# Kernel optimization log

Measured on AMD Instinct MI355X. Metric: run time of the kernel, lower is better.

Reference implementation:

```python
import jax, jax.numpy as jnp
import numpy as np
from jax import lax

ACT_BITS = 8
O, C, K = 256, 128, 3
STRIDE, PAD = 1, 1


def setup_inputs() -> dict:
    key = jax.random.key(0)
    kx, kw = jax.random.split(key)
    x = jax.random.uniform(kx, (16, C, 56, 56), dtype=jnp.float32)
    weight = jax.random.normal(kw, (O, C, K, K), dtype=jnp.float32)
    wrange = 2 ** 8  # weight_bits
    qw = jnp.clip(jnp.round(weight * (wrange - 1)), 0, wrange - 1)
    # PCILT: pcilt[o,c,kh,kw,i] = qw[o,c,kh,kw] * i  for i in [0, 2^act_bits)
    A = 2 ** ACT_BITS
    pcilt = qw[..., None] * jnp.arange(A, dtype=jnp.float32)  # [O,C,K,K,A]
    bias = jnp.zeros((O,), dtype=jnp.float32)
    return {"x": x, "pcilt": pcilt, "bias": bias}


def reference(x, pcilt, bias):
    A = pcilt.shape[-1]
    # quantize activations to integer LUT indices in [0, A-1]
    xq = jnp.clip(jnp.round(x * (A - 1)), 0.0, A - 1.0)
    # The gather-and-sum  out[b,o,h,w] = sum_{c,kh,kw} pcilt[o,c,kh,kw, idx]
    # is mathematically identical to a conv with qw = pcilt[...,1] applied to the
    # (float-cast) quantized indices, since pcilt[...,i] == qw * i exactly.
    qw = pcilt[..., 1]  # [O,C,K,K] quantized weights
    out = lax.conv_general_dilated(
        xq, qw,
        window_strides=(STRIDE, STRIDE),
        padding=((PAD, PAD), (PAD, PAD)),
        dimension_numbers=("NCHW", "OIHW", "NCHW"),
    )
    return out + bias[None, :, None, None]
```

## Files before the change

kernel.cpp:

```cpp
#include <hip/hip_runtime.h>
#include <stdint.h>

typedef unsigned short u16;
typedef __bf16 bf16x8 __attribute__((ext_vector_type(8)));
typedef float f32x4 __attribute__((ext_vector_type(4)));
typedef unsigned short u16x4 __attribute__((ext_vector_type(4)));
typedef unsigned short u16x8 __attribute__((ext_vector_type(8)));

#define B_N   16
#define C_CH  128
#define O_CH  256
#define HW    56
#define PH    58
#define PW    72
#define NCG   16

#define GLOBAL_AS __attribute__((address_space(1)))
#define LDS_AS    __attribute__((address_space(3)))

__device__ __forceinline__ void glds16(const u16* g, u16* l) {
    __builtin_amdgcn_global_load_lds((const GLOBAL_AS void*)g, (LDS_AS void*)l, 16, 0, 0);
}

__global__ __launch_bounds__(256) void quant_pad(const float* __restrict__ x,
                                                 u16* __restrict__ xq) {
    __shared__ u16 Lt[C_CH][57];
    const int hp = blockIdx.x;
    const int b = blockIdx.y;
    const int tid = threadIdx.x;
    const int h = hp - 1;
    const bool interior = (unsigned)h < HW;

    if (interior) {
        const float* xr = x + ((size_t)b * C_CH * HW + h) * HW;
        for (int i = 0; i < 7; ++i) {
            int u = i * 256 + tid;
            int c = u / 14, w4 = u % 14;
            float4 v = *(const float4*)(xr + (size_t)c * (HW * HW) + w4 * 4);
            float q0 = fminf(fmaxf(rintf(v.x * 255.0f), 0.0f), 255.0f);
            float q1 = fminf(fmaxf(rintf(v.y * 255.0f), 0.0f), 255.0f);
            float q2 = fminf(fmaxf(rintf(v.z * 255.0f), 0.0f), 255.0f);
            float q3 = fminf(fmaxf(rintf(v.w * 255.0f), 0.0f), 255.0f);
            Lt[c][w4 * 4 + 0] = (u16)(__float_as_uint(q0) >> 16);
            Lt[c][w4 * 4 + 1] = (u16)(__float_as_uint(q1) >> 16);
            Lt[c][w4 * 4 + 2] = (u16)(__float_as_uint(q2) >> 16);
            Lt[c][w4 * 4 + 3] = (u16)(__float_as_uint(q3) >> 16);
        }
    }
    __syncthreads();
    u16* dst = xq + (size_t)(b * PH + hp) * (NCG * PW * 8);
    for (int j = 0; j < 9; ++j) {
        int u = j * 256 + tid;
        int c8b = (u & 1) * 4;
        int wp = (u >> 1) % PW;
        int cg = u / (2 * PW);
        int w = wp - 1;
        u16x4 v = (u16x4){0, 0, 0, 0};
        if (interior && (unsigned)w < HW) {
#pragma unroll
            for (int e = 0; e < 4; ++e) v[e] = Lt[cg * 8 + c8b + e][w];
        }
        *(u16x4*)(dst + (size_t)u * 4) = v;
    }
}

__global__ __launch_bounds__(256) void make_w(const float* __restrict__ pcilt,
                                              u16* __restrict__ Bw) {
    int u = blockIdx.x * 256 + threadIdx.x;
    int o = u & 255;
    int cg = (u >> 8) & 15;
    int r = u >> 12;
    const float* src = pcilt + ((size_t)(o * C_CH + cg * 8) * 9 + r) * 256 + 1;
    u16x8 v;
#pragma unroll
    for (int e = 0; e < 8; ++e)
        v[e] = (u16)(__float_as_uint(src[(size_t)e * (9 * 256)]) >> 16);
    *(u16x8*)(Bw + (size_t)u * 8) = v;
}

__global__ __launch_bounds__(256) void conv_mfma(const u16* __restrict__ xq,
                                                 const u16* __restrict__ Bw,
                                                 const float* __restrict__ bias,
                                                 float* __restrict__ out) {
    __shared__ __align__(16) u16 Is[8][128][8];

    const int tid = threadIdx.x;
    const int o_blk = blockIdx.x * 128;
    const int h0 = blockIdx.y * 2;
    const int b = blockIdx.z;

    const int lane = tid & 63;
    const int wid = tid >> 6;
    const int wo = wid & 1;
    const int wm = wid >> 1;
    const int quad = lane >> 4;
    const int lrow = lane & 15;

    f32x4 acc[4][4];
#pragma unroll
    for (int i = 0; i < 4; i++)
#pragma unroll
        for (int j = 0; j < 4; j++) acc[i][j] = (f32x4){0.f, 0.f, 0.f, 0.f};

    const u16* wbase = Bw + (size_t)(o_blk + wo * 64 + lrow) * 8;

    for (int r = 0; r < 9; ++r) {
        const int kh = r / 3, kw = r % 3;
#pragma unroll
        for (int half = 0; half < 2; ++half) {
            __syncthreads();
#pragma unroll
            for (int gg = 0; gg < 2; ++gg) {
                const int g = wid + gg * 4;
                const int cg = half * 8 + g;
#pragma unroll
                for (int dh = 0; dh < 2; ++dh) {
                    const u16* src = xq +
                        ((size_t)((b * PH + h0 + dh + kh) * NCG + cg) * PW + kw + lane) * 8;
                    glds16(src, &Is[g][dh * 64][0]);
                }
            }
            bf16x8 af[2][4];
#pragma unroll
            for (int s = 0; s < 2; ++s) {
                const int cgw = r * 16 + half * 8 + s * 4 + quad;
#pragma unroll
                for (int i = 0; i < 4; ++i)
                    af[s][i] = *(const bf16x8*)(wbase + ((size_t)cgw * 256 + i * 16) * 8);
            }
            __syncthreads();
            bf16x8 bfr[2][4];
#pragma unroll
            for (int s = 0; s < 2; ++s)
#pragma unroll
                for (int j = 0; j < 4; ++j)
                    bfr[s][j] = *(const bf16x8*)&Is[s * 4 + quad][wm * 64 + j * 16 + lrow][0];
#pragma unroll
            for (int s = 0; s < 2; ++s)
#pragma unroll
                for (int i = 0; i < 4; ++i)
#pragma unroll
                    for (int j = 0; j < 4; ++j)
                        acc[i][j] = __builtin_amdgcn_mfma_f32_16x16x32_bf16(af[s][i], bfr[s][j], acc[i][j], 0, 0, 0);
        }
    }

    const int hh = h0 + wm;
#pragma unroll
    for (int i = 0; i < 4; i++) {
        const int obase = o_blk + wo * 64 + i * 16 + quad * 4;
#pragma unroll
        for (int j = 0; j < 4; j++) {
            const int w = j * 16 + lrow;
            if (w < HW) {
#pragma unroll
                for (int rg = 0; rg < 4; ++rg) {
                    const int o = obase + rg;
                    out[(((size_t)b * O_CH + o) * HW + hh) * HW + w] = acc[i][j][rg] + bias[o];
                }
            }
        }
    }
}

extern "C" void kernel_launch(void* const* d_in, const int* in_sizes, int n_in,
                              void* d_out, int out_size, void* d_ws, size_t ws_size,
                              hipStream_t stream) {
    const float* x     = (const float*)d_in[0];
    const float* pcilt = (const float*)d_in[1];
    const float* bias  = (const float*)d_in[2];
    float* out = (float*)d_out;

    u16* xq = (u16*)d_ws;
    u16* Bw = xq + (size_t)B_N * PH * NCG * PW * 8;

    quant_pad<<<dim3(PH, B_N), 256, 0, stream>>>(x, xq);
    make_w<<<(9 * NCG * O_CH * 8) / (8 * 256), 256, 0, stream>>>(pcilt, Bw);
    conv_mfma<<<dim3(O_CH / 128, HW / 2, B_N), dim3(256), 0, stream>>>(xq, Bw, bias, out);
}
```

Before: 411.1 us.

## Stage halo input rows in LDS once and reuse across all 9 taps

Restructures the conv loop so each half of the channel groups loads a 4-row by 72-column padded input halo into LDS once, then iterates all 9 kernel taps by offsetting LDS reads. This replaces 18 rounds of global->LDS loads and barriers with 2. It also double-buffers the weight fragments in registers, prefetching the next tap's weights before issuing the current tap's MFMAs. The cost is more LDS (about 37KB vs 16KB) and higher register pressure from two weight fragment buffers.

```diff
diff --git a/kernel.cpp b/kernel.cpp
--- a/kernel.cpp
+++ b/kernel.cpp
@@ -82,7 +82,7 @@
                                                  const u16* __restrict__ Bw,
                                                  const float* __restrict__ bias,
                                                  float* __restrict__ out) {
-    __shared__ __align__(16) u16 Is[8][128][8];
+    __shared__ __align__(16) u16 Ld[4][8][PW][8];
 
     const int tid = threadIdx.x;
     const int o_blk = blockIdx.x * 128;
@@ -102,46 +102,53 @@
 #pragma unroll
         for (int j = 0; j < 4; j++) acc[i][j] = (f32x4){0.f, 0.f, 0.f, 0.f};
 
-    const u16* wbase = Bw + (size_t)(o_blk + wo * 64 + lrow) * 8;
+    const u16* wl = Bw + (size_t)(o_blk + wo * 64 + lrow) * 8;
+    const u16* gsrc_row = xq + (size_t)((b * PH + h0 + wid) * NCG) * (PW * 8) + lane * 8;
+    u16* ldst_row = &Ld[wid][0][0][0];
 
-    for (int r = 0; r < 9; ++r) {
-        const int kh = r / 3, kw = r % 3;
+    for (int half = 0; half < 2; ++half) {
+        __syncthreads();
+        {
+            const u16* gs = gsrc_row + half * 8 * (PW * 8);
 #pragma unroll
-        for (int half = 0; half < 2; ++half) {
-            __syncthreads();
+            for (int k = 0; k < 9; ++k)
+                glds16(gs + k * 512, ldst_row + k * 512);
+        }
+        __syncthreads();
+
+        bf16x8 af[2][2][4];
 #pragma unroll
-            for (int gg = 0; gg < 2; ++gg) {
-                const int g = wid + gg * 4;
-                const int cg = half * 8 + g;
+        for (int s = 0; s < 2; ++s) {
+            const size_t base = (size_t)((0 * 16 + half * 8 + s * 4 + quad) * 256) * 8;
 #pragma unroll
-                for (int dh = 0; dh < 2; ++dh) {
-                    const u16* src = xq +
-                        ((size_t)((b * PH + h0 + dh + kh) * NCG + cg) * PW + kw + lane) * 8;
-                    glds16(src, &Is[g][dh * 64][0]);
+            for (int i = 0; i < 4; ++i)
+                af[0][s][i] = *(const bf16x8*)(wl + base + (size_t)i * 16 * 8);
+        }
+
+#pragma unroll
+        for (int r = 0; r < 9; ++r) {
+            if (r < 8) {
+#pragma unroll
+                for (int s = 0; s < 2; ++s) {
+                    const size_t base = (size_t)(((r + 1) * 16 + half * 8 + s * 4 + quad) * 256) * 8;
+#pragma unroll
+                    for (int i = 0; i < 4; ++i)
+                        af[(r + 1) & 1][s][i] = *(const bf16x8*)(wl + base + (size_t)i * 16 * 8);
                 }
             }
-            bf16x8 af[2][4];
+            const int kh = r / 3, kw = r % 3;
 #pragma unroll
             for (int s = 0; s < 2; ++s) {
-                const int cgw = r * 16 + half * 8 + s * 4 + quad;
-#pragma unroll
-                for (int i = 0; i < 4; ++i)
-                    af[s][i] = *(const bf16x8*)(wbase + ((size_t)cgw * 256 + i * 16) * 8);
-            }
-            __syncthreads();
-            bf16x8 bfr[2][4];
-#pragma unroll
-            for (int s = 0; s < 2; ++s)
+                bf16x8 bfr[4];
 #pragma unroll
                 for (int j = 0; j < 4; ++j)
-                    bfr[s][j] = *(const bf16x8*)&Is[s * 4 + quad][wm * 64 + j * 16 + lrow][0];
-#pragma unroll
-            for (int s = 0; s < 2; ++s)
+                    bfr[j] = *(const bf16x8*)&Ld[wm + kh][s * 4 + quad][kw + j * 16 + lrow][0];
 #pragma unroll
                 for (int i = 0; i < 4; ++i)
 #pragma unroll
                     for (int j = 0; j < 4; ++j)
-                        acc[i][j] = __builtin_amdgcn_mfma_f32_16x16x32_bf16(af[s][i], bfr[s][j], acc[i][j], 0, 0, 0);
+                        acc[i][j] = __builtin_amdgcn_mfma_f32_16x16x32_bf16(af[r & 1][s][i], bfr[j], acc[i][j], 0, 0, 0);
+            }
         }
     }
 
```

After: 426.9 us. +3.9%, slower.

## Stage input rows once per channel group with double-buffered LDS and weight prefetch

Applied to the files above, without the earlier changes.

The conv kernel now loads four padded input rows per channel quarter into LDS once and reuses them across all nine kernel taps. Before, the input tile was reloaded from global memory for every tap and half. The LDS tile is double-buffered so the next quarter's loads overlap compute, and weight fragments are prefetched one tap ahead. make_w is reworked so each thread writes two values and the launch uses more threads. An occupancy hint is also added. These changes cut redundant global-to-LDS traffic and barriers, at the cost of more LDS per block.

```diff
diff --git a/kernel.cpp b/kernel.cpp
--- a/kernel.cpp
+++ b/kernel.cpp
@@ -4,8 +4,8 @@
 typedef unsigned short u16;
 typedef __bf16 bf16x8 __attribute__((ext_vector_type(8)));
 typedef float f32x4 __attribute__((ext_vector_type(4)));
+typedef unsigned short u16x2 __attribute__((ext_vector_type(2)));
 typedef unsigned short u16x4 __attribute__((ext_vector_type(4)));
-typedef unsigned short u16x8 __attribute__((ext_vector_type(8)));
 
 #define B_N   16
 #define C_CH  128
@@ -66,23 +66,23 @@
 
 __global__ __launch_bounds__(256) void make_w(const float* __restrict__ pcilt,
                                               u16* __restrict__ Bw) {
-    int u = blockIdx.x * 256 + threadIdx.x;
-    int o = u & 255;
-    int cg = (u >> 8) & 15;
-    int r = u >> 12;
-    const float* src = pcilt + ((size_t)(o * C_CH + cg * 8) * 9 + r) * 256 + 1;
-    u16x8 v;
-#pragma unroll
-    for (int e = 0; e < 8; ++e)
-        v[e] = (u16)(__float_as_uint(src[(size_t)e * (9 * 256)]) >> 16);
-    *(u16x8*)(Bw + (size_t)u * 8) = v;
+    int v = blockIdx.x * 256 + threadIdx.x;
+    int e2 = v & 3;
+    int o  = (v >> 2) & 255;
+    int cg = (v >> 10) & 15;
+    int r  = v >> 14;
+    const float* src = pcilt + ((size_t)(o * C_CH + cg * 8 + e2 * 2) * 9 + r) * 256 + 1;
+    u16x2 out2;
+    out2[0] = (u16)(__float_as_uint(src[0]) >> 16);
+    out2[1] = (u16)(__float_as_uint(src[(size_t)9 * 256]) >> 16);
+    *(u16x2*)(Bw + (size_t)v * 2) = out2;
 }
 
-__global__ __launch_bounds__(256) void conv_mfma(const u16* __restrict__ xq,
-                                                 const u16* __restrict__ Bw,
-                                                 const float* __restrict__ bias,
-                                                 float* __restrict__ out) {
-    __shared__ __align__(16) u16 Is[8][128][8];
+__global__ __launch_bounds__(256, 3) void conv_mfma(const u16* __restrict__ xq,
+                                                    const u16* __restrict__ Bw,
+                                                    const float* __restrict__ bias,
+                                                    float* __restrict__ out) {
+    __shared__ __align__(16) u16 Ld[2][4][4][PW][8];
 
     const int tid = threadIdx.x;
     const int o_blk = blockIdx.x * 128;
@@ -102,46 +102,50 @@
 #pragma unroll
         for (int j = 0; j < 4; j++) acc[i][j] = (f32x4){0.f, 0.f, 0.f, 0.f};
 
-    const u16* wbase = Bw + (size_t)(o_blk + wo * 64 + lrow) * 8;
+    const u16* wl = Bw + (size_t)(o_blk + wo * 64 + lrow) * 8;
+    const u16* gsrow = xq + ((size_t)((b * PH + h0 + wid) * NCG) * PW) * 8 + lane * 8;
 
-    for (int r = 0; r < 9; ++r) {
-        const int kh = r / 3, kw = r % 3;
+#define STAGE(q, t)                                                         \
+    {                                                                       \
+        const u16* gs = gsrow + (size_t)((q) * 4) * (PW * 8);               \
+        u16* ld = &Ld[t][wid][0][0][0];                                     \
+        _Pragma("unroll")                                                   \
+        for (int oo = 0; oo < 4; ++oo) {                                    \
+            glds16(gs + oo * 576, ld + oo * 576);                           \
+            glds16(gs + oo * 576 + 64, ld + oo * 576 + 64);                 \
+        }                                                                   \
+    }
+
+#define LOAD_AF(slot, q, r)                                                 \
+    {                                                                       \
+        const size_t base = (size_t)(((r) * 16 + (q) * 4 + quad) * 256) * 8;\
+        _Pragma("unroll")                                                   \
+        for (int i = 0; i < 4; ++i)                                         \
+            af[slot][i] = *(const bf16x8*)(wl + base + (size_t)i * 16 * 8); \
+    }
+
+    STAGE(0, 0);
+    bf16x8 af[2][4];
+
 #pragma unroll
-        for (int half = 0; half < 2; ++half) {
-            __syncthreads();
+    for (int q = 0; q < 4; ++q) {
+        const int t = q & 1;
+        __syncthreads();
+        if (q < 3) STAGE(q + 1, t ^ 1);
+        LOAD_AF(0, q, 0);
 #pragma unroll
-            for (int gg = 0; gg < 2; ++gg) {
-                const int g = wid + gg * 4;
-                const int cg = half * 8 + g;
+        for (int r = 0; r < 9; ++r) {
+            if (r < 8) LOAD_AF((r + 1) & 1, q, r + 1);
+            const int kh = r / 3, kw = r % 3;
+            bf16x8 bfr[4];
 #pragma unroll
-                for (int dh = 0; dh < 2; ++dh) {
-                    const u16* src = xq +
-                        ((size_t)((b * PH + h0 + dh + kh) * NCG + cg) * PW + kw + lane) * 8;
-                    glds16(src, &Is[g][dh * 64][0]);
-                }
-            }
-            bf16x8 af[2][4];
+            for (int j = 0; j < 4; ++j)
+                bfr[j] = *(const bf16x8*)&Ld[t][wm + kh][quad][kw + j * 16 + lrow][0];
 #pragma unroll
-            for (int s = 0; s < 2; ++s) {
-                const int cgw = r * 16 + half * 8 + s * 4 + quad;
-#pragma unroll
-                for (int i = 0; i < 4; ++i)
-                    af[s][i] = *(const bf16x8*)(wbase + ((size_t)cgw * 256 + i * 16) * 8);
-            }
-            __syncthreads();
-            bf16x8 bfr[2][4];
-#pragma unroll
-            for (int s = 0; s < 2; ++s)
+            for (int i = 0; i < 4; ++i)
 #pragma unroll
                 for (int j = 0; j < 4; ++j)
-                    bfr[s][j] = *(const bf16x8*)&Is[s * 4 + quad][wm * 64 + j * 16 + lrow][0];
-#pragma unroll
-            for (int s = 0; s < 2; ++s)
-#pragma unroll
-                for (int i = 0; i < 4; ++i)
-#pragma unroll
-                    for (int j = 0; j < 4; ++j)
-                        acc[i][j] = __builtin_amdgcn_mfma_f32_16x16x32_bf16(af[s][i], bfr[s][j], acc[i][j], 0, 0, 0);
+                    acc[i][j] = __builtin_amdgcn_mfma_f32_16x16x32_bf16(af[r & 1][i], bfr[j], acc[i][j], 0, 0, 0);
         }
     }
 
@@ -175,6 +179,6 @@
     u16* Bw = xq + (size_t)B_N * PH * NCG * PW * 8;
 
     quant_pad<<<dim3(PH, B_N), 256, 0, stream>>>(x, xq);
-    make_w<<<(9 * NCG * O_CH * 8) / (8 * 256), 256, 0, stream>>>(pcilt, Bw);
+    make_w<<<(9 * NCG * O_CH * 4) / 256, 256, 0, stream>>>(pcilt, Bw);
     conv_mfma<<<dim3(O_CH / 128, HW / 2, B_N), dim3(256), 0, stream>>>(xq, Bw, bias, out);
 }
```

Result: slower. 422.9 us (+2.9%).

## Switch conv to int8 MFMA with offset-corrected signed operands

Applied to the files above, without the earlier changes.

Activations and weights are stored as unsigned bytes XOR 0x80, which makes them signed int8 values shifted by -128. The convolution then runs on i32 16x16x64 int8 MFMA instead of bf16. Per-pixel 3x3 window sums of activations and per-channel weight sums are precomputed, and the epilogue adds them back to undo the offset. This halves operand bytes and the MFMA instruction count, at the cost of extra small reduction kernels, atomics, and a more complex epilogue.

```diff
diff --git a/kernel.cpp b/kernel.cpp
--- a/kernel.cpp
+++ b/kernel.cpp
@@ -1,11 +1,10 @@
 #include <hip/hip_runtime.h>
 #include <stdint.h>
 
+typedef unsigned char u8;
 typedef unsigned short u16;
-typedef __bf16 bf16x8 __attribute__((ext_vector_type(8)));
-typedef float f32x4 __attribute__((ext_vector_type(4)));
-typedef unsigned short u16x4 __attribute__((ext_vector_type(4)));
-typedef unsigned short u16x8 __attribute__((ext_vector_type(8)));
+typedef int i32x4 __attribute__((ext_vector_type(4)));
+typedef u8 u8x4 __attribute__((ext_vector_type(4)));
 
 #define B_N   16
 #define C_CH  128
@@ -13,17 +12,24 @@
 #define HW    56
 #define PH    58
 #define PW    72
-#define NCG   16
 
 #define GLOBAL_AS __attribute__((address_space(1)))
 #define LDS_AS    __attribute__((address_space(3)))
 
-__device__ __forceinline__ void glds16(const u16* g, u16* l) {
+__device__ __forceinline__ void glds16(const void* g, void* l) {
     __builtin_amdgcn_global_load_lds((const GLOBAL_AS void*)g, (LDS_AS void*)l, 16, 0, 0);
 }
 
+#define XQ_OFF   0
+#define BW_OFF   8552448
+#define TC_OFF   (BW_OFF + 294912)
+#define SA_OFF   (TC_OFF + 267264)
+#define WS_OFF   (SA_OFF + 229376)
+
 __global__ __launch_bounds__(256) void quant_pad(const float* __restrict__ x,
-                                                 u16* __restrict__ xq) {
+                                                 u8* __restrict__ xq,
+                                                 int* __restrict__ Tc,
+                                                 int* __restrict__ Wsum) {
     __shared__ u16 Lt[C_CH][57];
     const int hp = blockIdx.x;
     const int b = blockIdx.y;
@@ -31,58 +37,100 @@
     const int h = hp - 1;
     const bool interior = (unsigned)h < HW;
 
+    if (hp == 0 && b == 0 && tid < 256) Wsum[tid] = 0;
+
     if (interior) {
         const float* xr = x + ((size_t)b * C_CH * HW + h) * HW;
         for (int i = 0; i < 7; ++i) {
             int u = i * 256 + tid;
             int c = u / 14, w4 = u % 14;
             float4 v = *(const float4*)(xr + (size_t)c * (HW * HW) + w4 * 4);
-            float q0 = fminf(fmaxf(rintf(v.x * 255.0f), 0.0f), 255.0f);
-            float q1 = fminf(fmaxf(rintf(v.y * 255.0f), 0.0f), 255.0f);
-            float q2 = fminf(fmaxf(rintf(v.z * 255.0f), 0.0f), 255.0f);
-            float q3 = fminf(fmaxf(rintf(v.w * 255.0f), 0.0f), 255.0f);
-            Lt[c][w4 * 4 + 0] = (u16)(__float_as_uint(q0) >> 16);
-            Lt[c][w4 * 4 + 1] = (u16)(__float_as_uint(q1) >> 16);
-            Lt[c][w4 * 4 + 2] = (u16)(__float_as_uint(q2) >> 16);
-            Lt[c][w4 * 4 + 3] = (u16)(__float_as_uint(q3) >> 16);
+            Lt[c][w4 * 4 + 0] = (u16)(int)fminf(fmaxf(rintf(v.x * 255.0f), 0.0f), 255.0f);
+            Lt[c][w4 * 4 + 1] = (u16)(int)fminf(fmaxf(rintf(v.y * 255.0f), 0.0f), 255.0f);
+            Lt[c][w4 * 4 + 2] = (u16)(int)fminf(fmaxf(rintf(v.z * 255.0f), 0.0f), 255.0f);
+            Lt[c][w4 * 4 + 3] = (u16)(int)fminf(fmaxf(rintf(v.w * 255.0f), 0.0f), 255.0f);
         }
     }
     __syncthreads();
-    u16* dst = xq + (size_t)(b * PH + hp) * (NCG * PW * 8);
+    u8* dst = xq + (size_t)(b * PH + hp) * 9216;
     for (int j = 0; j < 9; ++j) {
         int u = j * 256 + tid;
-        int c8b = (u & 1) * 4;
-        int wp = (u >> 1) % PW;
-        int cg = u / (2 * PW);
+        int d4 = u & 3;
+        int wp = (u >> 2) % PW;
+        int cg = u / (4 * PW);
         int w = wp - 1;
-        u16x4 v = (u16x4){0, 0, 0, 0};
+        u8x4 v;
         if (interior && (unsigned)w < HW) {
 #pragma unroll
-            for (int e = 0; e < 4; ++e) v[e] = Lt[cg * 8 + c8b + e][w];
-        }
-        *(u16x4*)(dst + (size_t)u * 4) = v;
+            for (int e = 0; e < 4; ++e)
+                v[e] = (u8)Lt[cg * 16 + d4 * 4 + e][w] ^ 0x80;
+        } else {
+            v = (u8x4){0x80, 0x80, 0x80, 0x80};
+        }
+        *(u8x4*)(dst + (size_t)u * 4) = v;
+    }
+    if (tid < PW) {
+        int wp = tid, w = wp - 1;
+        int s = -128 * C_CH;
+        if (interior && (unsigned)w < HW) {
+            for (int c = 0; c < C_CH; ++c) s += (int)Lt[c][w];
+        }
+        Tc[(b * PH + hp) * PW + wp] = s;
     }
 }
 
 __global__ __launch_bounds__(256) void make_w(const float* __restrict__ pcilt,
-                                              u16* __restrict__ Bw) {
-    int u = blockIdx.x * 256 + threadIdx.x;
-    int o = u & 255;
-    int cg = (u >> 8) & 15;
-    int r = u >> 12;
-    const float* src = pcilt + ((size_t)(o * C_CH + cg * 8) * 9 + r) * 256 + 1;
-    u16x8 v;
-#pragma unroll
-    for (int e = 0; e < 8; ++e)
-        v[e] = (u16)(__float_as_uint(src[(size_t)e * (9 * 256)]) >> 16);
-    *(u16x8*)(Bw + (size_t)u * 8) = v;
-}
-
-__global__ __launch_bounds__(256) void conv_mfma(const u16* __restrict__ xq,
-                                                 const u16* __restrict__ Bw,
+                                              u8* __restrict__ Bw,
+                                              const int* __restrict__ Tc,
+                                              int* __restrict__ Sa,
+                                              int* __restrict__ Wsum) {
+    const int bx = blockIdx.x;
+    const int tid = threadIdx.x;
+    if (bx < 288) {
+        int v = bx * 256 + tid;
+        int cb4 = v & 15;
+        int o   = (v >> 4) & 255;
+        int q   = (v >> 12) & 1;
+        int r   = v >> 13;
+        u8x4 out4;
+        int part = 0;
+#pragma unroll
+        for (int e = 0; e < 4; ++e) {
+            int c = q * 64 + cb4 * 4 + e;
+            float w = pcilt[((size_t)(o * C_CH + c) * 9 + r) * 256 + 1];
+            int qi = (int)w;
+            out4[e] = (u8)qi ^ 0x80;
+            part += qi - 128;
+        }
+        *(u8x4*)(Bw + (size_t)v * 4) = out4;
+        part += __shfl_down(part, 1);
+        part += __shfl_down(part, 2);
+        part += __shfl_down(part, 4);
+        part += __shfl_down(part, 8);
+        if ((tid & 15) == 0) atomicAdd(&Wsum[o], part);
+    } else {
+        int sidx = (bx - 288) * 256 + tid;
+        int w = sidx % HW;
+        int h = (sidx / HW) % HW;
+        int b = sidx / (HW * HW);
+        const int* t = Tc + (b * PH + h) * PW + w;
+        int s = 0;
+#pragma unroll
+        for (int dh = 0; dh < 3; ++dh)
+#pragma unroll
+            for (int dw = 0; dw < 3; ++dw)
+                s += t[dh * PW + dw];
+        Sa[(b * HW + h) * 64 + w] = s;
+    }
+}
+
+__global__ __launch_bounds__(256) void conv_mfma(const u8* __restrict__ xq,
+                                                 const u8* __restrict__ Bw,
+                                                 const int* __restrict__ Sa,
+                                                 const int* __restrict__ Wsum,
                                                  const float* __restrict__ bias,
                                                  float* __restrict__ out) {
-    __shared__ __align__(16) u16 Is[8][128][8];
+    __shared__ __align__(16) u8 Is[4][128][16];
 
     const int tid = threadIdx.x;
     const int o_blk = blockIdx.x * 128;
@@ -96,67 +144,67 @@
     const int quad = lane >> 4;
     const int lrow = lane & 15;
 
-    f32x4 acc[4][4];
+    i32x4 acc[4][4];
 #pragma unroll
     for (int i = 0; i < 4; i++)
 #pragma unroll
-        for (int j = 0; j < 4; j++) acc[i][j] = (f32x4){0.f, 0.f, 0.f, 0.f};
-
-    const u16* wbase = Bw + (size_t)(o_blk + wo * 64 + lrow) * 8;
+        for (int j = 0; j < 4; j++) acc[i][j] = (i32x4){0, 0, 0, 0};
+
+    const int sdh = wid & 1;
+    const int scg = (wid >> 1) * 2;
+    const u8* gbase = xq + (size_t)(b * PH + h0 + sdh) * 9216 + lane * 16;
+    const u8* wl = Bw + (size_t)(o_blk + wo * 64 + lrow) * 64 + quad * 16;
 
     for (int r = 0; r < 9; ++r) {
         const int kh = r / 3, kw = r % 3;
 #pragma unroll
-        for (int half = 0; half < 2; ++half) {
+        for (int q = 0; q < 2; ++q) {
+            const int st = r * 2 + q;
             __syncthreads();
 #pragma unroll
-            for (int gg = 0; gg < 2; ++gg) {
-                const int g = wid + gg * 4;
-                const int cg = half * 8 + g;
-#pragma unroll
-                for (int dh = 0; dh < 2; ++dh) {
-                    const u16* src = xq +
-                        ((size_t)((b * PH + h0 + dh + kh) * NCG + cg) * PW + kw + lane) * 8;
-                    glds16(src, &Is[g][dh * 64][0]);
-                }
+            for (int cc = 0; cc < 2; ++cc) {
+                const int cg = scg + cc;
+                const u8* src = gbase + (size_t)kh * 9216 + (q * 4 + cg) * (PW * 16) + kw * 16;
+                glds16(src, &Is[cg][sdh * 64][0]);
             }
-            bf16x8 af[2][4];
-#pragma unroll
-            for (int s = 0; s < 2; ++s) {
-                const int cgw = r * 16 + half * 8 + s * 4 + quad;
-#pragma unroll
-                for (int i = 0; i < 4; ++i)
-                    af[s][i] = *(const bf16x8*)(wbase + ((size_t)cgw * 256 + i * 16) * 8);
-            }
+            i32x4 af[4];
+#pragma unroll
+            for (int i = 0; i < 4; ++i)
+                af[i] = *(const i32x4*)(wl + ((size_t)st * 256 + i * 16) * 64);
             __syncthreads();
-            bf16x8 bfr[2][4];
-#pragma unroll
-            for (int s = 0; s < 2; ++s)
+            i32x4 bfr[4];
+#pragma unroll
+            for (int j = 0; j < 4; ++j)
+                bfr[j] = *(const i32x4*)&Is[quad][wm * 64 + j * 16 + lrow][0];
+#pragma unroll
+            for (int i = 0; i < 4; ++i)
 #pragma unroll
                 for (int j = 0; j < 4; ++j)
-                    bfr[s][j] = *(const bf16x8*)&Is[s * 4 + quad][wm * 64 + j * 16 + lrow][0];
-#pragma unroll
-            for (int s = 0; s < 2; ++s)
-#pragma unroll
-                for (int i = 0; i < 4; ++i)
-#pragma unroll
-                    for (int j = 0; j < 4; ++j)
-                        acc[i][j] = __builtin_amdgcn_mfma_f32_16x16x32_bf16(af[s][i], bfr[s][j], acc[i][j], 0, 0, 0);
+                    acc[i][j] = __builtin_amdgcn_mfma_i32_16x16x64_i8(af[i], bfr[j], acc[i][j], 0, 0, 0);
         }
     }
 
     const int hh = h0 + wm;
+    int sa_j[4];
+#pragma unroll
+    for (int j = 0; j < 4; ++j) {
+        const int w = j * 16 + lrow;
+        sa_j[j] = (w < HW) ? Sa[(b * HW + hh) * 64 + w] : 0;
+    }
 #pragma unroll
     for (int i = 0; i < 4; i++) {
         const int obase = o_blk + wo * 64 + i * 16 + quad * 4;
 #pragma unroll
-        for (int j = 0; j < 4; j++) {
-            const int w = j * 16 + lrow;
-            if (w < HW) {
-#pragma unroll
-                for (int rg = 0; rg < 4; ++rg) {
-                    const int o = obase + rg;
-                    out[(((size_t)b * O_CH + o) * HW + hh) * HW + w] = acc[i][j][rg] + bias[o];
+        for (int rg = 0; rg < 4; ++rg) {
+            const int o = obase + rg;
+            const int wsum = Wsum[o];
+            const float bs = bias[o];
+#pragma unroll
+            for (int j = 0; j < 4; ++j) {
+                const int w = j * 16 + lrow;
+                if (w < HW) {
+                    int tot = acc[i][j][rg] + 128 * (sa_j[j] + wsum) + 18874368;
+                    out[(((size_t)b * O_CH + o) * HW + hh) * HW + w] = (float)tot + bs;
                 }
             }
         }
@@ -171,10 +219,14 @@
     const float* bias  = (const float*)d_in[2];
     float* out = (float*)d_out;
 
-    u16* xq = (u16*)d_ws;
-    u16* Bw = xq + (size_t)B_N * PH * NCG * PW * 8;
-
-    quant_pad<<<dim3(PH, B_N), 256, 0, stream>>>(x, xq);
-    make_w<<<(9 * NCG * O_CH * 8) / (8 * 256), 256, 0, stream>>>(pcilt, Bw);
-    conv_mfma<<<dim3(O_CH / 128, HW / 2, B_N), dim3(256), 0, stream>>>(xq, Bw, bias, out);
-}
+    u8* ws = (u8*)d_ws;
+    u8*  xq   = ws + XQ_OFF;
+    u8*  Bw   = ws + BW_OFF;
+    int* Tc   = (int*)(ws + TC_OFF);
+    int* Sa   = (int*)(ws + SA_OFF);
+    int* Wsum = (int*)(ws + WS_OFF);
+
+    quant_pad<<<dim3(PH, B_N), 256, 0, stream>>>(x, xq, Tc, Wsum);
+    make_w<<<484, 256, 0, stream>>>(pcilt, Bw, Tc, Sa, Wsum);
+    conv_mfma<<<dim3(O_CH / 128, HW / 2, B_N), dim3(256), 0, stream>>>(xq, Bw, Sa, Wsum, bias, out);
+}
```

Result: no change. 406.2 us (-1.2%).
